# Kernel optimization log

Measured on AMD Instinct MI355X. Metric: run time of the kernel, lower is better.

The kernel has to match this reference:

```python
import jax, jax.numpy as jnp
import numpy as np

C64 = jnp.complex64


def _ry(t):  # scalar angle -> [2,2] complex
    c = jnp.cos(t / 2).astype(C64)
    s = jnp.sin(t / 2).astype(C64)
    return jnp.stack([jnp.stack([c, -s]), jnp.stack([s, c])])


def _rz(t):  # scalar angle -> [2,2] complex (diagonal)
    p = jnp.exp(-0.5j * t.astype(C64))
    z = jnp.zeros((), C64)
    return jnp.stack([jnp.stack([p, z]), jnp.stack([z, jnp.conj(p)])])


def _rx_batch(t):  # t: [B] -> [B,2,2] complex (per-sample RX encoding gate)
    c = jnp.cos(t / 2).astype(C64)
    s = jnp.sin(t / 2).astype(C64)
    row0 = jnp.stack([c, -1j * s], axis=-1)
    row1 = jnp.stack([-1j * s, c], axis=-1)
    return jnp.stack([row0, row1], axis=-2)


def _apply_1q(state, gate, wire, n):
    # state: [B, 2^n]; wire 0 is the most significant bit (PennyLane convention)
    B = state.shape[0]
    pre, post = 2 ** wire, 2 ** (n - wire - 1)
    s = state.reshape(B, pre, 2, post)
    if gate.ndim == 2:
        s = jnp.einsum('ij,bpjq->bpiq', gate, s)
    else:  # per-sample gate [B,2,2]
        s = jnp.einsum('bij,bpjq->bpiq', gate, s)
    return s.reshape(B, -1)


def _apply_cnot(state, wire, n):
    # CNOT with control=wire, target=wire+1 (adjacent wires)
    B = state.shape[0]
    pre, post = 2 ** wire, 2 ** (n - wire - 2)
    s = state.reshape(B, pre, 2, 2, post)
    # control==1 block gets its target axis flipped
    s = jnp.concatenate([s[:, :, :1], s[:, :, 1:, ::-1]], axis=2)
    return s.reshape(B, -1)


def _circuit(x, params):
    # Batched statevector simulation of: RX(x_i) encoding, then n_layers of
    # (RY,RZ,RY) per wire + CNOT chain, then <Z_i> per wire.
    B, n = x.shape
    L = params.shape[0]
    state = jnp.zeros((B, 2 ** n), C64).at[:, 0].set(1.0)
    for i in range(n):
        state = _apply_1q(state, _rx_batch(x[:, i]), i, n)
    for l in range(L):
        for i in range(n):
            # RY(p0) first, then RZ(p1), then RY(p2): fuse into one 2x2 gate
            g = _ry(params[l, i, 2]) @ _rz(params[l, i, 1]) @ _ry(params[l, i, 0])
            state = _apply_1q(state, g, i, n)
        for i in range(n - 1):
            state = _apply_cnot(state, i, n)
    probs = jnp.abs(state) ** 2  # [B, 2^n] float32
    ez = []
    for i in range(n):
        p = probs.reshape(B, 2 ** i, 2, 2 ** (n - i - 1))
        ez.append(p[:, :, 0].sum((1, 2)) - p[:, :, 1].sum((1, 2)))
    return jnp.stack(ez, axis=1)  # [B, n]


def setup_inputs() -> dict:
    key = jax.random.key(0)
    k1, k2, k3, _ = jax.random.split(key, 4)
    B, n, L = 8192, 12, 3
    return {
        'x': jax.random.normal(k1, (B, n), jnp.float32),
        'params': jax.random.normal(k2, (L, n, 3), jnp.float32),
        'head_w': jax.random.normal(k3, (1, n), jnp.float32) / np.float32(np.sqrt(n)),
        'head_b': jnp.zeros((1,), jnp.float32),
    }


def reference(x, params, head_w, head_b):
    ez = _circuit(x, params)           # [B, n] per-wire Z expectations
    out = ez @ head_w.T + head_b       # Linear(n, 1)
    return out[:, 0]                   # squeeze(-1) -> [B]
```

## Files before the change

### kernel.cpp

```cpp
#include <hip/hip_runtime.h>
#include <math.h>

#define NQ 12
#define NTH 256
#define NL 3
#define GRID 768

typedef _Float16 h8 __attribute__((ext_vector_type(8)));
typedef _Float16 h4 __attribute__((ext_vector_type(4)));
typedef _Float16 hf2 __attribute__((ext_vector_type(2)));
typedef float f4 __attribute__((ext_vector_type(4)));

#define MFMA __builtin_amdgcn_mfma_f32_16x16x32_f16


__device__ __forceinline__ int swzf(int off) {
    return off ^ (((((off >> 6) ^ (off >> 9)) & 7)) << 3);
}
__device__ __forceinline__ int swz1(int off) {
    return off ^ ((((off >> 5) ^ (off >> 9)) & 7) << 3);
}
__device__ __forceinline__ int swzw(int off) {
    return off ^ (((off >> 6) & 7) << 3);
}

__device__ __forceinline__ unsigned pk2(float lo, float hi) {
    hf2 t_; t_.x = (_Float16)lo; t_.y = (_Float16)hi;
    unsigned r_; __builtin_memcpy(&r_, &t_, 4); return r_;
}

__device__ __forceinline__ h8 xition(f4 re, f4 im) {
    unsigned a0 = pk2(re.x, re.y), a1 = pk2(re.z, re.w);
    unsigned b0 = pk2(im.x, im.y), b1 = pk2(im.z, im.w);
    asm("v_permlane32_swap_b32 %0, %1" : "+v"(a0), "+v"(b0));
    asm("v_permlane16_swap_b32 %0, %1" : "+v"(a0), "+v"(b0));
    asm("v_permlane32_swap_b32 %0, %1" : "+v"(a1), "+v"(b1));
    asm("v_permlane16_swap_b32 %0, %1" : "+v"(a1), "+v"(b1));
    union { unsigned u[4]; h8 v; } r_;
    r_.u[0] = a0; r_.u[1] = a1; r_.u[2] = b0; r_.u[3] = b1;
    return r_.v;
}

__global__ void __launch_bounds__(NTH, 3)
qsim_kernel(const float* __restrict__ x,
            const float* __restrict__ params,
            const float* __restrict__ head_w,
            const float* __restrict__ head_b,
            float* __restrict__ out, int Btot) {
    __shared__ __align__(16) _Float16 Sst[16384];
    __shared__ __align__(16) _Float16 Wl[9216];
    __shared__ float wlo[64], whi[64];
    __shared__ float csx[6 * 24], snx[6 * 24];
    __shared__ float wred[8];
    float* Gs = (float*)Sst;

    const int t = threadIdx.x, blk = blockIdx.x;
    const int npairs = (Btot + 1) >> 1;

    if (t < 36) {
        float p0 = params[t * 3 + 0], p1 = params[t * 3 + 1], p2 = params[t * 3 + 2];
        float c0 = cosf(0.5f * p0), s0 = sinf(0.5f * p0);
        float ch = cosf(0.5f * p1), sh = sinf(0.5f * p1);
        float c2 = cosf(0.5f * p2), s2 = sinf(0.5f * p2);
        float pr_ = ch, pi = -sh, qr = ch, qi = sh;
        float A = c2 * c0, Bc = s2 * s0, Cc = c2 * s0, D = s2 * c0;
        float* g = &Gs[t * 8];
        g[0] = A * pr_ - Bc * qr;  g[1] = A * pi - Bc * qi;
        g[2] = -Cc * pr_ - D * qr; g[3] = -Cc * pi - D * qi;
        g[4] = D * pr_ + Cc * qr;  g[5] = D * pi + Cc * qi;
        g[6] = -Bc * pr_ + A * qr; g[7] = -Bc * pi + A * qi;
    }
    if (t >= 36 && t < 180) {
        int idx = t - 36;
        int pr = idx / 24, w = idx - pr * 24;
        int pairIdx = blk + pr * GRID;
        if (pairIdx < npairs) {
            int smp = pairIdx * 2 + (w >= 12 ? 1 : 0);
            int wire = (w >= 12) ? (w - 12) : w;
            if (smp < Btot) {
                float xv = 0.5f * x[smp * NQ + wire];
                csx[pr * 24 + w] = cosf(xv);
                snx[pr * 24 + w] = sinf(xv);
            }
        }
    }
    if (t >= 192) {
        int v = t - 192; float s = 0.f, s2 = 0.f;
#pragma unroll
        for (int be = 0; be < 6; ++be) {
            s  += ((v >> be) & 1) ? -head_w[11 - be] : head_w[11 - be];
            s2 += ((v >> be) & 1) ? -head_w[5 - be]  : head_w[5 - be];
        }
        wlo[v] = s; whi[v] = s2;
    }
    __syncthreads();

#pragma unroll
    for (int i = 0; i < 36; ++i) {
        int e = i * 256 + t;
        int s = e >> 10, idx = e & 1023;
        int n = idx >> 5, k = idx & 31;
        int rp = n >> 4, tp = n & 15, rr = k >> 4, tt = k & 15;
        int l = s / 3, g = s - 3 * l;
        float ur = 1.f, ui = 0.f;
#pragma unroll
        for (int jj = 0; jj < 4; ++jj) {
            int wire = 11 - (4 * g + jj);
            const float* gp = &Gs[(l * 12 + wire) * 8];
            int rb = (tp >> jj) & 1, cb = (tt >> jj) & 1;
            float gr = gp[(rb * 2 + cb) * 2], gi = gp[(rb * 2 + cb) * 2 + 1];
            float nr = ur * gr - ui * gi;
            float ni = ur * gi + ui * gr;
            ur = nr; ui = ni;
        }
        float val = (rp == 0) ? ((rr == 0) ? ur : -ui)
                              : ((rr == 0) ? ui : ur);
        Wl[swzw(e)] = (_Float16)val;
    }
    __syncthreads();

    const int wv = t >> 6, u = t & 15, q = (t >> 4) & 3;
    const int wbs = swzw(u * 32 + q * 8);
    int g0b[4], g1b[4];
#pragma unroll
    for (int mb = 0; mb < 4; ++mb) {
        int m_ = wv * 64 + (u >> 2) * 16 + mb * 4 + (u & 3);
        g0b[mb] = swzf(m_ * 32 + q * 8);
        int l_ = t & 63;
        int m1 = ((l_ >> 2) & 3) * 64 + (l_ & 3) * 16 + wv * 4 + mb;
        g1b[mb] = swz1(m1 * 32 + q * 8);
    }
    const int sb = (t * 32) ^ (((t ^ (t >> 4)) & 7) << 3);

    const int s4 = (u ^ (u >> 1) ^ (u >> 2) ^ (u >> 3)) & 15;
    const int P4 = s4 & 1, q0 = q & 1, q1 = q >> 1;
    const int j7 = q1 ^ P4, j6 = q0 ^ q1 ^ P4;
    const int wv0 = wv & 1, wv1 = wv >> 1;
    int Eo[4], PwR[4];
#pragma unroll
    for (int r = 0; r < 4; ++r) {
        int r0 = r & 1, r1 = r >> 1;
        int j5 = r1 ^ j6, j4 = (r0 ^ r1) ^ j6;
        int j3 = wv1 ^ j4, j2 = wv0 ^ wv1 ^ j4;
        int m0 = s4 * 16 + j7 * 8 + j6 * 4 + j5 * 2 + j4;
        Eo[r]  = swzf(m0 * 32 + j3 * 8 + j2 * 4);
        PwR[r] = (wv0 ^ wv1 ^ j4);
    }
    const int Pw0 = wv0 ^ wv1 ^ j6;
    const int wloB = j6 * 48 + (wv1 ^ j6) * 8 + (wv0 ^ wv1 ^ j6) * 4 + Pw0 * 3;
    const float whiv = whi[s4 * 4 + j7 * 2 + j6];
    const f4 Z = {0.f, 0.f, 0.f, 0.f};

#define ST16(off_, va_, vb_) { h8 w_;                                        \
    w_[0] = (_Float16)(va_).x; w_[1] = (_Float16)(va_).y;                    \
    w_[2] = (_Float16)(va_).z; w_[3] = (_Float16)(va_).w;                    \
    w_[4] = (_Float16)(vb_).x; w_[5] = (_Float16)(vb_).y;                    \
    w_[6] = (_Float16)(vb_).z; w_[7] = (_Float16)(vb_).w;                    \
    *(h8*)&Sst[off_] = w_; }

#define PST1(CMP_, r_) {                                                     \
    bool pw_ = PwR[r_] != 0;                                                 \
    { float v0=eRA[0].CMP_, v1=eRA[1].CMP_, v2=eRA[2].CMP_, v3=eRA[3].CMP_;  \
      h4 w_; w_.x=(_Float16)(pw_?v2:v0); w_.y=(_Float16)(pw_?v3:v1);         \
             w_.z=(_Float16)(pw_?v1:v3); w_.w=(_Float16)(pw_?v0:v2);         \
      *(h4*)&Sst[Eo[r_]] = w_; }                                             \
    { float v0=eIA[0].CMP_, v1=eIA[1].CMP_, v2=eIA[2].CMP_, v3=eIA[3].CMP_;  \
      h4 w_; w_.x=(_Float16)(pw_?v2:v0); w_.y=(_Float16)(pw_?v3:v1);         \
             w_.z=(_Float16)(pw_?v1:v3); w_.w=(_Float16)(pw_?v0:v2);         \
      *(h4*)&Sst[Eo[r_] ^ 16] = w_; }                                        \
    { float v0=eRB[0].CMP_, v1=eRB[1].CMP_, v2=eRB[2].CMP_, v3=eRB[3].CMP_;  \
      h4 w_; w_.x=(_Float16)(pw_?v2:v0); w_.y=(_Float16)(pw_?v3:v1);         \
             w_.z=(_Float16)(pw_?v1:v3); w_.w=(_Float16)(pw_?v0:v2);         \
      *(h4*)&Sst[Eo[r_] + 8192] = w_; }                                      \
    { float v0=eIB[0].CMP_, v1=eIB[1].CMP_, v2=eIB[2].CMP_, v3=eIB[3].CMP_;  \
      h4 w_; w_.x=(_Float16)(pw_?v2:v0); w_.y=(_Float16)(pw_?v3:v1);         \
             w_.z=(_Float16)(pw_?v1:v3); w_.w=(_Float16)(pw_?v0:v2);         \
      *(h4*)&Sst[(Eo[r_] ^ 16) + 8192] = w_; } }

#define RD1(CMP_, dr_) {                                                     \
    int b_ = wloB ^ (dr_);                                                   \
    float w0_ = whiv + wlo[b_],     w1_ = whiv + wlo[b_ ^ 1];                \
    float w2_ = whiv + wlo[b_ ^ 3], w3_ = whiv + wlo[b_ ^ 2];                \
    racc0 = fmaf(fmaf(eRA[0].CMP_, eRA[0].CMP_, eIA[0].CMP_*eIA[0].CMP_), w0_, racc0); \
    racc0 = fmaf(fmaf(eRA[1].CMP_, eRA[1].CMP_, eIA[1].CMP_*eIA[1].CMP_), w1_, racc0); \
    racc0 = fmaf(fmaf(eRA[2].CMP_, eRA[2].CMP_, eIA[2].CMP_*eIA[2].CMP_), w2_, racc0); \
    racc0 = fmaf(fmaf(eRA[3].CMP_, eRA[3].CMP_, eIA[3].CMP_*eIA[3].CMP_), w3_, racc0); \
    racc1 = fmaf(fmaf(eRB[0].CMP_, eRB[0].CMP_, eIB[0].CMP_*eIB[0].CMP_), w0_, racc1); \
    racc1 = fmaf(fmaf(eRB[1].CMP_, eRB[1].CMP_, eIB[1].CMP_*eIB[1].CMP_), w1_, racc1); \
    racc1 = fmaf(fmaf(eRB[2].CMP_, eRB[2].CMP_, eIB[2].CMP_*eIB[2].CMP_), w2_, racc1); \
    racc1 = fmaf(fmaf(eRB[3].CMP_, eRB[3].CMP_, eIB[3].CMP_*eIB[3].CMP_), w3_, racc1); }

#define INITS(cs_, sn_, SOFF_) {                                             \
    int m_ = t;                                                              \
    float magm_ = 1.f;                                                       \
    _Pragma("unroll") for (int j_ = 0; j_ < 8; ++j_)                         \
        magm_ *= ((m_ >> j_) & 1) ? (sn_)[7 - j_] : (cs_)[7 - j_];           \
    float A2_[4], B2_[4];                                                    \
    _Pragma("unroll") for (int v_ = 0; v_ < 4; ++v_) {                       \
        A2_[v_] = ((v_ & 1) ? (sn_)[11] : (cs_)[11]) *                       \
                  ((v_ & 2) ? (sn_)[10] : (cs_)[10]);                        \
        B2_[v_] = ((v_ & 1) ? (sn_)[9] : (cs_)[9]) *                         \
                  ((v_ & 2) ? (sn_)[8] : (cs_)[8]);                          \
    }                                                                        \
    int pm_ = __popc(m_);                                                    \
    _Pragma("unroll") for (int reim_ = 0; reim_ < 2; ++reim_) {              \
        h8 w0_, w1_;                                                         \
        _Pragma("unroll") for (int tau_ = 0; tau_ < 16; ++tau_) {            \
            float mag_ = magm_ * A2_[tau_ & 3] * B2_[tau_ >> 2];             \
            int p_ = (pm_ + __popc(tau_)) & 3;                               \
            bool nz_ = ((p_ & 1) == reim_);                                  \
            bool ng_ = ((((p_ >> 1) & 1) ^ reim_) != 0);                     \
            float v_ = nz_ ? (ng_ ? -mag_ : mag_) : 0.f;                     \
            if (tau_ < 8) w0_[tau_] = (_Float16)v_; else w1_[tau_ - 8] = (_Float16)v_; \
        }                                                                    \
        int off_ = m_ * 32 + reim_ * 16;                                     \
        *(h8*)&Sst[swzf(off_) + (SOFF_)] = w0_;                              \
        *(h8*)&Sst[swzf(off_ + 8) + (SOFF_)] = w1_;                          \
    } }

#pragma unroll 1
    for (int pr = 0; ; ++pr) {
        const int pairIdx = blk + pr * GRID;
        if (pairIdx >= npairs) break;
        const float* cs0 = &csx[pr * 24];
        const float* sn0 = &snx[pr * 24];
        INITS(cs0, sn0, 0)
        INITS((cs0 + 12), (sn0 + 12), 8192)
        __syncthreads();

        float racc0 = 0.f, racc1 = 0.f;
#pragma unroll
        for (int l = 0; l < NL; ++l) {
            {
                const int sW = (l * 3 + 0) * 1024;
                h8 bf0 = *(const h8*)&Wl[sW + wbs];
                h8 bf1 = *(const h8*)&Wl[sW + 512 + wbs];
                h8 aA[4], aB[4];
#pragma unroll
                for (int mb = 0; mb < 4; ++mb) {
                    aA[mb] = *(const h8*)&Sst[g0b[mb]];
                    aB[mb] = *(const h8*)&Sst[g0b[mb] + 8192];
                }
                __syncthreads();
                f4 cR[4], cI[4];
#pragma unroll
                for (int mb = 0; mb < 4; ++mb) {
                    cR[mb] = MFMA(aA[mb], bf0, Z, 0, 0, 0);
                    cI[mb] = MFMA(aA[mb], bf1, Z, 0, 0, 0);
                }
                ST16(sb,        cR[0], cR[1]) ST16(sb ^ 8,  cR[2], cR[3])
                ST16(sb ^ 16,   cI[0], cI[1]) ST16(sb ^ 24, cI[2], cI[3])
#pragma unroll
                for (int mb = 0; mb < 4; ++mb) {
                    cR[mb] = MFMA(aB[mb], bf0, Z, 0, 0, 0);
                    cI[mb] = MFMA(aB[mb], bf1, Z, 0, 0, 0);
                }
                ST16(sb + 8192,        cR[0], cR[1]) ST16((sb ^ 8) + 8192,  cR[2], cR[3])
                ST16((sb ^ 16) + 8192, cI[0], cI[1]) ST16((sb ^ 24) + 8192, cI[2], cI[3])
                __syncthreads();
            }
            {
                const int sW1 = (l * 3 + 1) * 1024, sW2 = (l * 3 + 2) * 1024;
                h8 bg0 = *(const h8*)&Wl[sW1 + wbs];
                h8 bg1 = *(const h8*)&Wl[sW1 + 512 + wbs];
                h8 bh0 = *(const h8*)&Wl[sW2 + wbs];
                h8 bh1 = *(const h8*)&Wl[sW2 + 512 + wbs];
                h8 gA[4], gB[4];
#pragma unroll
                for (int mb = 0; mb < 4; ++mb) {
                    gA[mb] = *(const h8*)&Sst[g1b[mb]];
                    gB[mb] = *(const h8*)&Sst[g1b[mb] + 8192];
                }
                if (l < NL - 1) __syncthreads();
                f4 eRA[4], eIA[4], eRB[4], eIB[4];
                {
                    f4 dR[4], dI[4]; h8 t2[4];
#pragma unroll
                    for (int mb = 0; mb < 4; ++mb) {
                        dR[mb] = MFMA(gA[mb], bg0, Z, 0, 0, 0);
                        dI[mb] = MFMA(gA[mb], bg1, Z, 0, 0, 0);
                    }
#pragma unroll
                    for (int mb = 0; mb < 4; ++mb) t2[mb] = xition(dR[mb], dI[mb]);
#pragma unroll
                    for (int mb = 0; mb < 4; ++mb) {
                        eRA[mb] = MFMA(t2[mb], bh0, Z, 0, 0, 0);
                        eIA[mb] = MFMA(t2[mb], bh1, Z, 0, 0, 0);
                    }
                }
                {
                    f4 dR[4], dI[4]; h8 t2[4];
#pragma unroll
                    for (int mb = 0; mb < 4; ++mb) {
                        dR[mb] = MFMA(gB[mb], bg0, Z, 0, 0, 0);
                        dI[mb] = MFMA(gB[mb], bg1, Z, 0, 0, 0);
                    }
#pragma unroll
                    for (int mb = 0; mb < 4; ++mb) t2[mb] = xition(dR[mb], dI[mb]);
#pragma unroll
                    for (int mb = 0; mb < 4; ++mb) {
                        eRB[mb] = MFMA(t2[mb], bh0, Z, 0, 0, 0);
                        eIB[mb] = MFMA(t2[mb], bh1, Z, 0, 0, 0);
                    }
                }
                if (l < NL - 1) {
                    PST1(x, 0) PST1(y, 1) PST1(z, 2) PST1(w, 3)
                    __syncthreads();
                } else {
                    RD1(x, 0) RD1(y, 31) RD1(z, 63) RD1(w, 32)
                }
            }
        }
#pragma unroll
        for (int o = 32; o >= 1; o >>= 1) {
            racc0 += __shfl_xor(racc0, o, 64);
            racc1 += __shfl_xor(racc1, o, 64);
        }
        if ((t & 63) == 0) { wred[wv] = racc0; wred[4 + wv] = racc1; }
        __syncthreads();
        if (t < 2) {
            int smp = pairIdx * 2 + t;
            if (smp < Btot) {
                float r = head_b[0];
#pragma unroll
                for (int i2 = 0; i2 < 4; ++i2) r += wred[t * 4 + i2];
                out[smp] = r;
            }
        }
    }
}

extern "C" void kernel_launch(void* const* d_in, const int* in_sizes, int n_in,
                              void* d_out, int out_size, void* d_ws, size_t ws_size,
                              hipStream_t stream) {
    const float* x = (const float*)d_in[0];
    const float* params = (const float*)d_in[1];
    const float* head_w = (const float*)d_in[2];
    const float* head_b = (const float*)d_in[3];
    float* out = (float*)d_out;
    int B = in_sizes[0] / NQ;

    hipLaunchKernelGGL(qsim_kernel, dim3(GRID), dim3(NTH), 0, stream,
                       x, params, head_w, head_b, out, B);
}
```

Baseline: 121.2 us.

## Fold encoding and first variational layer into analytic product-state initialization

The RX encoding followed by the first layer of single-qubit rotations (before any CNOT) leaves a product state, so each wire's 2-vector is computed directly and the initial state is built as a product of per-group factors. This removes the first layer's three MFMA gate stages with their LDS round-trips and barriers, and shrinks the gate-matrix LDS buffer from 9 to 6 stages. In exchange it adds a small per-pair factor computation, an extra barrier, and a Gray-code indexing scheme that must match the existing swizzled layout exactly.

```diff
diff --git a/kernel.cpp b/kernel.cpp
--- a/kernel.cpp
+++ b/kernel.cpp
@@ -14,6 +14,10 @@
 #define MFMA __builtin_amdgcn_mfma_f32_16x16x32_f16
 
 
+__device__ __forceinline__ int sfx(int v) {
+    v ^= v >> 1; v ^= v >> 2; v ^= v >> 4; v ^= v >> 8;
+    return v;
+}
 __device__ __forceinline__ int swzf(int off) {
     return off ^ (((((off >> 6) ^ (off >> 9)) & 7)) << 3);
 }
@@ -48,9 +52,11 @@
             const float* __restrict__ head_b,
             float* __restrict__ out, int Btot) {
     __shared__ __align__(16) _Float16 Sst[16384];
-    __shared__ __align__(16) _Float16 Wl[9216];
+    __shared__ __align__(16) _Float16 Wl[6144];
     __shared__ float wlo[64], whi[64];
     __shared__ float csx[6 * 24], snx[6 * 24];
+    __shared__ float Gs0[96];
+    __shared__ __align__(16) float fct[2][48][2];
     __shared__ float wred[8];
     float* Gs = (float*)Sst;
 
@@ -95,12 +101,14 @@
     }
     __syncthreads();
 
-#pragma unroll
-    for (int i = 0; i < 36; ++i) {
+    if (t < 96) Gs0[t] = Gs[t];
+#pragma unroll
+    for (int i = 0; i < 24; ++i) {
         int e = i * 256 + t;
-        int s = e >> 10, idx = e & 1023;
+        int s = (e >> 10) + 3;
+        int idx = e & 1023;
         int n = idx >> 5, k = idx & 31;
-        int rp = n >> 4, tp = n & 15, rr = k >> 4, tt = k & 15;
+        int rp = n >> 4, tp = n & 15, rr = k >> 4, tt = k & 31 & 15;
         int l = s / 3, g = s - 3 * l;
         float ur = 1.f, ui = 0.f;
 #pragma unroll
@@ -150,6 +158,11 @@
     const int wloB = j6 * 48 + (wv1 ^ j6) * 8 + (wv0 ^ wv1 ^ j6) * 4 + Pw0 * 3;
     const float whiv = whi[s4 * 4 + j7 * 2 + j6];
     const f4 Z = {0.f, 0.f, 0.f, 0.f};
+
+    const int iu = (t ^ (t >> 1)) & 0xFF;
+    const int aI = iu >> 4;
+    const int bI = 16 + (iu & 15);
+    const int flip = (t & 1) << 3;
 
 #define ST16(off_, va_, vb_) { h8 w_;                                        \
     w_[0] = (_Float16)(va_).x; w_[1] = (_Float16)(va_).y;                    \
@@ -190,49 +203,68 @@
     racc1 = fmaf(fmaf(eRB[2].CMP_, eRB[2].CMP_, eIB[2].CMP_*eIB[2].CMP_), w2_, racc1); \
     racc1 = fmaf(fmaf(eRB[3].CMP_, eRB[3].CMP_, eIB[3].CMP_*eIB[3].CMP_), w3_, racc1); }
 
-#define INITS(cs_, sn_, SOFF_) {                                             \
-    int m_ = t;                                                              \
-    float magm_ = 1.f;                                                       \
-    _Pragma("unroll") for (int j_ = 0; j_ < 8; ++j_)                         \
-        magm_ *= ((m_ >> j_) & 1) ? (sn_)[7 - j_] : (cs_)[7 - j_];           \
-    float A2_[4], B2_[4];                                                    \
-    _Pragma("unroll") for (int v_ = 0; v_ < 4; ++v_) {                       \
-        A2_[v_] = ((v_ & 1) ? (sn_)[11] : (cs_)[11]) *                       \
-                  ((v_ & 2) ? (sn_)[10] : (cs_)[10]);                        \
-        B2_[v_] = ((v_ & 1) ? (sn_)[9] : (cs_)[9]) *                         \
-                  ((v_ & 2) ? (sn_)[8] : (cs_)[8]);                          \
-    }                                                                        \
-    int pm_ = __popc(m_);                                                    \
-    _Pragma("unroll") for (int reim_ = 0; reim_ < 2; ++reim_) {              \
-        h8 w0_, w1_;                                                         \
-        _Pragma("unroll") for (int tau_ = 0; tau_ < 16; ++tau_) {            \
-            float mag_ = magm_ * A2_[tau_ & 3] * B2_[tau_ >> 2];             \
-            int p_ = (pm_ + __popc(tau_)) & 3;                               \
-            bool nz_ = ((p_ & 1) == reim_);                                  \
-            bool ng_ = ((((p_ >> 1) & 1) ^ reim_) != 0);                     \
-            float v_ = nz_ ? (ng_ ? -mag_ : mag_) : 0.f;                     \
-            if (tau_ < 8) w0_[tau_] = (_Float16)v_; else w1_[tau_ - 8] = (_Float16)v_; \
-        }                                                                    \
-        int off_ = m_ * 32 + reim_ * 16;                                     \
-        *(h8*)&Sst[swzf(off_) + (SOFF_)] = w0_;                              \
-        *(h8*)&Sst[swzf(off_ + 8) + (SOFF_)] = w1_;                          \
-    } }
-
 #pragma unroll 1
     for (int pr = 0; ; ++pr) {
         const int pairIdx = blk + pr * GRID;
         if (pairIdx >= npairs) break;
-        const float* cs0 = &csx[pr * 24];
-        const float* sn0 = &snx[pr * 24];
-        INITS(cs0, sn0, 0)
-        INITS((cs0 + 12), (sn0 + 12), 8192)
+
+        if (t < 96) {
+            int s_ = t / 48, k_ = t - s_ * 48;
+            int grp = k_ >> 4, h = k_ & 15;
+            int wbase = (grp == 0) ? 3 : (grp == 1) ? 7 : 11;
+            const float* cs_ = &csx[pr * 24 + s_ * 12];
+            const float* sn_ = &snx[pr * 24 + s_ * 12];
+            float ur = 1.f, ui = 0.f;
+#pragma unroll
+            for (int jj = 0; jj < 4; ++jj) {
+                int w = wbase - jj;
+                int bit = (h >> jj) & 1;
+                const float* g = &Gs0[w * 8];
+                float c = cs_[w], sn = sn_[w];
+                float tr, ti;
+                if (bit == 0) { tr = g[0] * c + g[3] * sn; ti = g[1] * c - g[2] * sn; }
+                else          { tr = g[4] * c + g[7] * sn; ti = g[5] * c - g[6] * sn; }
+                float nr = ur * tr - ui * ti, ni = ur * ti + ui * tr;
+                ur = nr; ui = ni;
+            }
+            fct[s_][k_][0] = ur; fct[s_][k_][1] = ui;
+        }
         __syncthreads();
 
+#pragma unroll
+        for (int s_ = 0; s_ < 2; ++s_) {
+            const int SOFF = s_ * 8192;
+            float ar = fct[s_][aI][0], ai = fct[s_][aI][1];
+            float br = fct[s_][bI][0], bi = fct[s_][bI][1];
+            float abr = ar * br - ai * bi, abi = ar * bi + ai * br;
+            float cr[16], ci[16];
+#pragma unroll
+            for (int k = 0; k < 16; ++k) {
+                cr[k] = fct[s_][32 + (k ^ flip)][0];
+                ci[k] = fct[s_][32 + (k ^ flip)][1];
+            }
+            h8 wr0, wr1, wi0, wi1;
+#pragma unroll
+            for (int tau = 0; tau < 16; ++tau) {
+                const int cidx = tau ^ (tau >> 1);
+                float vr = abr * cr[cidx] - abi * ci[cidx];
+                float vi = abr * ci[cidx] + abi * cr[cidx];
+                if (tau < 8) { wr0[tau] = (_Float16)vr; wi0[tau] = (_Float16)vi; }
+                else         { wr1[tau - 8] = (_Float16)vr; wi1[tau - 8] = (_Float16)vi; }
+            }
+            const int off0 = t * 32;
+            *(h8*)&Sst[swzf(off0)      + SOFF] = wr0;
+            *(h8*)&Sst[swzf(off0 + 8)  + SOFF] = wr1;
+            *(h8*)&Sst[swzf(off0 + 16) + SOFF] = wi0;
+            *(h8*)&Sst[swzf(off0 + 24) + SOFF] = wi1;
+        }
+        __syncthreads();
+
         float racc0 = 0.f, racc1 = 0.f;
 #pragma unroll
-        for (int l = 0; l < NL; ++l) {
+        for (int l = 1; l < NL; ++l) {
             {
-                const int sW = (l * 3 + 0) * 1024;
+                const int sW = ((l - 1) * 3 + 0) * 1024;
                 h8 bf0 = *(const h8*)&Wl[sW + wbs];
                 h8 bf1 = *(const h8*)&Wl[sW + 512 + wbs];
                 h8 aA[4], aB[4];
@@ -260,7 +292,7 @@
                 __syncthreads();
             }
             {
-                const int sW1 = (l * 3 + 1) * 1024, sW2 = (l * 3 + 2) * 1024;
+                const int sW1 = ((l - 1) * 3 + 1) * 1024, sW2 = ((l - 1) * 3 + 2) * 1024;
                 h8 bg0 = *(const h8*)&Wl[sW1 + wbs];
                 h8 bg1 = *(const h8*)&Wl[sW1 + 512 + wbs];
                 h8 bh0 = *(const h8*)&Wl[sW2 + wbs];
```

New measurement: 104.6 us. 13.7% less time.
